# Kernel tuning notes

Measured on AMD Instinct MI355X. Metric: run time of the kernel, lower is better.

## Reference

```python
import jax, jax.numpy as jnp
import numpy as np

H, D = 8, 16            # heads, per-head dim (hidden_channels // heads)
HID = H * D             # 128
N_MAT, N_ELEM = 100000, 118
F_MAT, F_ELEM = 128, 64
OUT = 64
E_EM, E_MM = 1000000, 2000000
NEG_SLOPE = 0.2

def _k(i):
    return jax.random.fold_in(jax.random.key(0), i)

def setup_inputs() -> dict:
    p = lambda i, shape: 0.1 * jax.random.normal(_k(i), shape, dtype=jnp.float32)
    return dict(
        x_mat=jax.random.normal(_k(0), (N_MAT, F_MAT), dtype=jnp.float32),
        x_elem=jax.random.normal(_k(1), (N_ELEM, F_ELEM), dtype=jnp.float32),
        W_proj_mat=p(2, (HID, F_MAT)), b_proj_mat=p(3, (HID,)),
        W_proj_elem=p(4, (HID, F_ELEM)), b_proj_elem=p(5, (HID,)),
        a_src_em=p(6, (H, D)), a_dst_em=p(7, (H, D)),
        a_src_mm=p(8, (H, D)), a_dst_mm=p(9, (H, D)),
        Wk=p(10, (HID, HID)), bk=p(11, (HID,)), q=p(12, (HID,)),
        Wl=p(13, (OUT, HID)), bl=p(14, (OUT,)),
        src_em=jax.random.randint(_k(15), (E_EM,), 0, N_ELEM, dtype=jnp.int32),
        dst_em=jax.random.randint(_k(16), (E_EM,), 0, N_MAT, dtype=jnp.int32),
        src_mm=jax.random.randint(_k(17), (E_MM,), 0, N_MAT, dtype=jnp.int32),
        dst_mm=jax.random.randint(_k(18), (E_MM,), 0, N_MAT, dtype=jnp.int32),
    )

def _edge_type_conv(x_s, x_d, a_s, a_d, src, dst, n_dst):
    # x_s:[Ns,H,D], x_d:[Nd,H,D]; per-edge-type GAT-style attention (HANConv.message)
    alpha = jnp.sum(x_s * a_s, -1)[src] + jnp.sum(x_d * a_d, -1)[dst]   # [E,H]
    alpha = jax.nn.leaky_relu(alpha, NEG_SLOPE)
    amax = jax.ops.segment_max(alpha, dst, num_segments=n_dst)          # stable softmax per dst
    ex = jnp.exp(alpha - amax[dst])
    den = jax.ops.segment_sum(ex, dst, num_segments=n_dst)
    w = ex / (den[dst] + 1e-16)                                         # [E,H]
    out = jax.ops.segment_sum(x_s[src] * w[:, :, None], dst, num_segments=n_dst)  # [Nd,H,D]
    return jax.nn.relu(out.reshape(n_dst, HID))

def _group(xs, q, Wk, bk):
    # HANConv semantic-level attention over metapaths
    s = jnp.stack(xs)                                                   # [M,N,C]
    score = jnp.sum(q * jnp.mean(jnp.tanh(s @ Wk.T + bk), axis=1), axis=-1)  # [M]
    attn = jax.nn.softmax(score)
    return jnp.einsum('m,mnc->nc', attn, s)

def reference(x_mat, x_elem, W_proj_mat, b_proj_mat, W_proj_elem, b_proj_elem,
              a_src_em, a_dst_em, a_src_mm, a_dst_mm, Wk, bk, q, Wl, bl,
              src_em, dst_em, src_mm, dst_mm):
    h_mat = (x_mat @ W_proj_mat.T + b_proj_mat).reshape(N_MAT, H, D)
    h_elem = (x_elem @ W_proj_elem.T + b_proj_elem).reshape(N_ELEM, H, D)
    o_em = _edge_type_conv(h_elem, h_mat, a_src_em, a_dst_em, src_em, dst_em, N_MAT)
    o_mm = _edge_type_conv(h_mat, h_mat, a_src_mm, a_dst_mm, src_mm, dst_mm, N_MAT)
    out_mat = _group([o_em, o_mm], q, Wk, bk)                           # [N_MAT, HID]
    return out_mat @ Wl.T + bl                                          # final Linear
```

## Files before the change

### kernel.cpp

```cpp
#include <hip/hip_runtime.h>
#include <hip/hip_bf16.h>

typedef unsigned int uint32;
typedef unsigned short ushort16;

using bf16x8 = __attribute__((ext_vector_type(8))) short;
using f32x4  = __attribute__((ext_vector_type(4))) float;

#define N_MATN 100000
#define N_ELEMN 118
#define F_MATN 128
#define F_ELEMN 64
#define HIDN 128
#define NHEAD 8
#define OUTC 64
#define NSTRIPS 6250
#define NT2 16
#define NTILES2 (N_MATN/NT2)

#define SH 8
#define NBK 391
#define BCH 8192

__device__ __forceinline__ float blo(uint32 u){ return __uint_as_float(u << 16); }
__device__ __forceinline__ float bhi(uint32 u){ return __uint_as_float(u & 0xffff0000u); }
__device__ __forceinline__ ushort16 f2bf(float f){
    uint32 u = __float_as_uint(f);
    uint32 r = u + 0x7FFFu + ((u >> 16) & 1u);
    return (ushort16)(r >> 16);
}
__device__ __forceinline__ uint32 pack2(float a, float b){
    return (uint32)f2bf(a) | ((uint32)f2bf(b) << 16);
}
__device__ __forceinline__ bf16x8 cvt8(const float* __restrict__ p){
    bf16x8 r;
    #pragma unroll
    for(int j=0;j<8;j++) r[j] = (short)f2bf(p[j]);
    return r;
}

__global__ __launch_bounds__(256) void proj_all(
    const float* __restrict__ xe, const float* __restrict__ We,
    const float* __restrict__ be, const float* __restrict__ a_se,
    ushort16* __restrict__ h_elem, float* __restrict__ asrc_em,
    const float* __restrict__ x, const float* __restrict__ W,
    const float* __restrict__ bias,
    const float* __restrict__ a_de, const float* __restrict__ a_sm, const float* __restrict__ a_dm,
    ushort16* __restrict__ h,
    float* __restrict__ adst_em, float* __restrict__ asrc_mm, float* __restrict__ adst_mm)
{
    __shared__ float xr[F_ELEMN];
    int tid = threadIdx.x;
    if(blockIdx.x < N_ELEMN){
        int n = blockIdx.x, c = tid;
        if(c < 16) ((float4*)xr)[c] = ((const float4*)(xe + n*F_ELEMN))[c];
        __syncthreads();
        if(c < 128){
            const float4* Wr = (const float4*)(We + c*F_ELEMN);
            float acc = 0.f;
            #pragma unroll 4
            for(int i=0;i<16;i++){
                float4 w = Wr[i];
                acc += xr[4*i]*w.x + xr[4*i+1]*w.y + xr[4*i+2]*w.z + xr[4*i+3]*w.w;
            }
            acc += be[c];
            h_elem[n*HIDN + c] = f2bf(acc);
            float p = acc * a_se[c];
            #pragma unroll
            for(int m=8;m>=1;m>>=1) p += __shfl_xor(p, m, 16);
            if((c&15)==0) asrc_em[n*NHEAD + (c>>4)] = p;
        }
        return;
    }
    int wv = tid >> 6, lane = tid & 63, quad = lane >> 4, sl = lane & 15;
    bf16x8 B[2][4];
    float bc[2], ade[2], asv[2], adv[2];
    #pragma unroll
    for(int i=0;i<2;i++){
        int c = (2*wv+i)*16 + sl;
        const float* wr = W + c*F_MATN;
        #pragma unroll
        for(int ks=0;ks<4;ks++) B[i][ks] = cvt8(wr + ks*32 + quad*8);
        bc[i] = bias[c]; ade[i] = a_de[c]; asv[i] = a_sm[c]; adv[i] = a_dm[c];
    }
    int nb = gridDim.x - N_ELEMN;
    for(int s = blockIdx.x - N_ELEMN; s < NSTRIPS; s += nb){
        int n0 = s*16;
        const float* xrow = x + (size_t)(n0+sl)*F_MATN;
        bf16x8 A[4];
        #pragma unroll
        for(int ks=0;ks<4;ks++) A[ks] = cvt8(xrow + ks*32 + quad*8);
        f32x4 acc[2];
        #pragma unroll
        for(int i=0;i<2;i++){ acc[i][0]=0.f; acc[i][1]=0.f; acc[i][2]=0.f; acc[i][3]=0.f; }
        #pragma unroll
        for(int i=0;i<2;i++)
            #pragma unroll
            for(int ks=0;ks<4;ks++)
                acc[i] = __builtin_amdgcn_mfma_f32_16x16x32_bf16(A[ks], B[i][ks], acc[i], 0, 0, 0);
        #pragma unroll
        for(int i=0;i<2;i++){
            int head = 2*wv + i;
            #pragma unroll
            for(int r=0;r<4;r++){
                float a = acc[i][r] + bc[i];
                int node = n0 + quad*4 + r;
                h[(size_t)node*HIDN + head*16 + sl] = f2bf(a);
                float p0 = a*ade[i], p1 = a*asv[i], p2 = a*adv[i];
                #pragma unroll
                for(int m=8;m>=1;m>>=1){
                    p0 += __shfl_xor(p0, m);
                    p1 += __shfl_xor(p1, m);
                    p2 += __shfl_xor(p2, m);
                }
                if(sl == 0){
                    adst_em[node*NHEAD + head] = p0;
                    asrc_mm[node*NHEAD + head] = p1;
                    adst_mm[node*NHEAD + head] = p2;
                }
            }
        }
    }
}

__global__ __launch_bounds__(256) void bucket_count(
    const int* __restrict__ dst_em, int nE_em, int* __restrict__ bcnt_em,
    const int* __restrict__ dst_mm, int nE_mm, int* __restrict__ bcnt_mm)
{
    __shared__ int he[NBK], hm[NBK];
    int t = threadIdx.x;
    for(int i=t;i<NBK;i+=256){ he[i]=0; hm[i]=0; }
    __syncthreads();
    int gt = blockIdx.x*256 + t;
    int st = gridDim.x*256;
    {
        int n4 = nE_em >> 2;
        const int4* d4 = (const int4*)dst_em;
        for(int i = gt; i < n4; i += st){
            int4 v = d4[i];
            atomicAdd(&he[v.x>>SH],1); atomicAdd(&he[v.y>>SH],1);
            atomicAdd(&he[v.z>>SH],1); atomicAdd(&he[v.w>>SH],1);
        }
        for(int i = (n4<<2) + gt; i < nE_em; i += st) atomicAdd(&he[dst_em[i]>>SH],1);
    }
    {
        int n4 = nE_mm >> 2;
        const int4* d4 = (const int4*)dst_mm;
        for(int i = gt; i < n4; i += st){
            int4 v = d4[i];
            atomicAdd(&hm[v.x>>SH],1); atomicAdd(&hm[v.y>>SH],1);
            atomicAdd(&hm[v.z>>SH],1); atomicAdd(&hm[v.w>>SH],1);
        }
        for(int i = (n4<<2) + gt; i < nE_mm; i += st) atomicAdd(&hm[dst_mm[i]>>SH],1);
    }
    __syncthreads();
    for(int j=t;j<NBK;j+=256){
        int a = he[j], b = hm[j];
        if(a) atomicAdd(&bcnt_em[j], a);
        if(b) atomicAdd(&bcnt_mm[j], b);
    }
}

__global__ __launch_bounds__(512) void bucket_scan(
    const int* __restrict__ bcnt_em, int* __restrict__ bb_em, int* __restrict__ bcur_em,
    const int* __restrict__ bcnt_mm, int* __restrict__ bb_mm, int* __restrict__ bcur_mm,
    int* __restrict__ offs_em, int* __restrict__ offs_mm, int nE_em, int nE_mm)
{
    __shared__ int wsum[8];
    int t = threadIdx.x, l = t & 63, w = t >> 6;
    {
        int v = (t < NBK) ? bcnt_em[t] : 0;
        int x = v;
        #pragma unroll
        for(int off=1; off<64; off<<=1){ int y = __shfl_up(x, off); if(l >= off) x += y; }
        if(l == 63) wsum[w] = x;
        __syncthreads();
        int base = 0;
        for(int k=0;k<w;k++) base += wsum[k];
        int excl = base + x - v;
        if(t < NBK){ bb_em[t] = excl; bcur_em[t] = excl; }
        if(t == 0){ bb_em[NBK] = nE_em; offs_em[N_MATN] = nE_em; }
        __syncthreads();
    }
    {
        int v = (t < NBK) ? bcnt_mm[t] : 0;
        int x = v;
        #pragma unroll
        for(int off=1; off<64; off<<=1){ int y = __shfl_up(x, off); if(l >= off) x += y; }
        if(l == 63) wsum[w] = x;
        __syncthreads();
        int base = 0;
        for(int k=0;k<w;k++) base += wsum[k];
        int excl = base + x - v;
        if(t < NBK){ bb_mm[t] = excl; bcur_mm[t] = excl; }
        if(t == 0){ bb_mm[NBK] = nE_mm; offs_mm[N_MATN] = nE_mm; }
    }
}

__global__ __launch_bounds__(256) void bin_pass(
    const int* __restrict__ src_em, const int* __restrict__ dst_em, int nE_em,
    int* __restrict__ bcur_em, uint32* __restrict__ st_em,
    const int* __restrict__ src_mm, const int* __restrict__ dst_mm, int nE_mm,
    int* __restrict__ bcur_mm, uint32* __restrict__ st_mm)
{
    __shared__ int cnt[NBK];
    __shared__ int base[NBK];
    int t = threadIdx.x;
    int nch_em = (nE_em + BCH - 1)/BCH;
    int nch_mm = (nE_mm + BCH - 1)/BCH;
    int ntot = nch_em + nch_mm;
    for(int c = blockIdx.x; c < ntot; c += gridDim.x){
        bool em = c < nch_em;
        const int* src = em ? src_em : src_mm;
        const int* dst = em ? dst_em : dst_mm;
        int nE   = em ? nE_em : nE_mm;
        int* bcur = em ? bcur_em : bcur_mm;
        uint32* st = em ? st_em : st_mm;
        int cc = em ? c : c - nch_em;
        int s = cc*BCH;
        int e = s + BCH; if(e > nE) e = nE;
        int len = e - s;
        int n4 = len >> 2;
        const int4* d4 = (const int4*)(dst + s);
        const int4* s4 = (const int4*)(src + s);
        for(int i=t;i<NBK;i+=256) cnt[i] = 0;
        __syncthreads();
        for(int i=t;i<n4;i+=256){
            int4 v = d4[i];
            atomicAdd(&cnt[v.x>>SH],1); atomicAdd(&cnt[v.y>>SH],1);
            atomicAdd(&cnt[v.z>>SH],1); atomicAdd(&cnt[v.w>>SH],1);
        }
        for(int i = s + (n4<<2) + t; i < e; i += 256) atomicAdd(&cnt[dst[i]>>SH], 1);
        __syncthreads();
        for(int i=t;i<NBK;i+=256){
            int v = cnt[i];
            base[i] = v ? atomicAdd(&bcur[i], v) : 0;
            cnt[i] = 0;
        }
        __syncthreads();
        for(int i=t;i<n4;i+=256){
            int4 dv = d4[i];
            int4 sv = s4[i];
            int b, p;
            b = dv.x>>SH; p = base[b] + atomicAdd(&cnt[b],1);
            st[p] = ((uint32)(dv.x & ((1<<SH)-1)) << 17) | (uint32)sv.x;
            b = dv.y>>SH; p = base[b] + atomicAdd(&cnt[b],1);
            st[p] = ((uint32)(dv.y & ((1<<SH)-1)) << 17) | (uint32)sv.y;
            b = dv.z>>SH; p = base[b] + atomicAdd(&cnt[b],1);
            st[p] = ((uint32)(dv.z & ((1<<SH)-1)) << 17) | (uint32)sv.z;
            b = dv.w>>SH; p = base[b] + atomicAdd(&cnt[b],1);
            st[p] = ((uint32)(dv.w & ((1<<SH)-1)) << 17) | (uint32)sv.w;
        }
        for(int i = s + (n4<<2) + t; i < e; i += 256){
            int d = dst[i];
            int b = d >> SH;
            int p = base[b] + atomicAdd(&cnt[b], 1);
            st[p] = ((uint32)(d & ((1<<SH)-1)) << 17) | (uint32)src[i];
        }
        __syncthreads();
    }
}

__global__ __launch_bounds__(256) void place_pass(
    const int* __restrict__ bb_em, const uint32* __restrict__ st_em,
    int* __restrict__ csr_em, int* __restrict__ offs_em,
    const int* __restrict__ bb_mm, const uint32* __restrict__ st_mm,
    int* __restrict__ csr_mm, int* __restrict__ offs_mm)
{
    __shared__ int cnt[256];
    __shared__ int wsum[4];
    __shared__ int cur[256];
    int b = blockIdx.x;
    bool em = b < NBK;
    const int* bb        = em ? bb_em : bb_mm;
    const uint32* stp    = em ? st_em : st_mm;
    int* csr             = em ? csr_em : csr_mm;
    int* offs            = em ? offs_em : offs_mm;
    int bk = em ? b : b - NBK;
    int d0 = bk << SH;
    int t = threadIdx.x, l = t & 63, w = t >> 6;
    int nd = N_MATN - d0; if(nd > 256) nd = 256;
    int beg = bb[bk], end = bb[bk+1];
    cnt[t] = 0;
    __syncthreads();
    for(int i = beg + t; i < end; i += 256)
        atomicAdd(&cnt[stp[i] >> 17], 1);
    __syncthreads();
    int v = cnt[t];
    int x = v;
    #pragma unroll
    for(int off=1; off<64; off<<=1){ int y = __shfl_up(x, off); if(l >= off) x += y; }
    if(l == 63) wsum[w] = x;
    __syncthreads();
    int base = beg;
    for(int k=0;k<w;k++) base += wsum[k];
    int excl = base + x - v;
    cur[t] = excl;
    if(t < nd) offs[d0 + t] = excl;
    __syncthreads();
    for(int i = beg + t; i < end; i += 256){
        uint32 vv = stp[i];
        int dl = (int)(vv >> 17);
        int p = atomicAdd(&cur[dl], 1);
        csr[p] = (int)(vv & 0x1FFFFu);
    }
}

__global__ __launch_bounds__(256) void agg_both(
    const int* __restrict__ offs_em, const int* __restrict__ csr_em,
    const ushort16* __restrict__ h_elem, const float* __restrict__ asrc_em,
    const float* __restrict__ adst_em, ushort16* __restrict__ o_em,
    const int* __restrict__ offs_mm, const int* __restrict__ csr_mm,
    const ushort16* __restrict__ h_mat, const float* __restrict__ asrc_mm,
    const float* __restrict__ adst_mm, ushort16* __restrict__ o_mm)
{
    int lane = threadIdx.x & 63;
    int g = lane >> 4;
    int q = lane & 15;
    int hd = q >> 1;
    int w = (blockIdx.x*blockDim.x + threadIdx.x) >> 6;
    int nw = (gridDim.x*blockDim.x) >> 6;

    int begN = 0, endN = 0; float adN = 0.f;
    if(w < 2*N_MATN){
        int nid0 = __builtin_amdgcn_readfirstlane(w);
        bool em0 = nid0 < N_MATN;
        int dx = em0 ? nid0 : nid0 - N_MATN;
        const int* offsx = em0 ? offs_em : offs_mm;
        const float* adpx = em0 ? adst_em : adst_mm;
        begN = offsx[dx]; endN = offsx[dx+1];
        adN = adpx[(unsigned)(dx*NHEAD + hd)];
    }

    for(int nid = w; nid < 2*N_MATN; nid += nw){
        int nidu = __builtin_amdgcn_readfirstlane(nid);
        bool em = nidu < N_MATN;
        int d = em ? nidu : nidu - N_MATN;
        const int*    csr  = em ? csr_em  : csr_mm;
        const uint32* hs   = (const uint32*)(em ? h_elem : h_mat);
        const float*  asp  = em ? asrc_em : asrc_mm;
        uint32*       op   = (uint32*)(em ? o_em : o_mm);
        int beg = begN, end = endN;
        float ad = adN;
        int nxt = nidu + nw;
        if(nxt < 2*N_MATN){
            bool emx = nxt < N_MATN;
            int dx = emx ? nxt : nxt - N_MATN;
            const int* offsx = emx ? offs_em : offs_mm;
            const float* adpx = emx ? adst_em : adst_mm;
            begN = offsx[dx]; endN = offsx[dx+1];
            adN = adpx[(unsigned)(dx*NHEAD + hd)];
        }
        float denA = 0.f, denB = 0.f;
        float nloA[4] = {0.f,0.f,0.f,0.f}, nhiA[4] = {0.f,0.f,0.f,0.f};
        float nloB[4] = {0.f,0.f,0.f,0.f}, nhiB[4] = {0.f,0.f,0.f,0.f};
        for(int j0 = beg; j0 < end; j0 += 8){
            int e0 = j0 + 2*g, e1 = e0 + 1;
            bool v0 = e0 < end, v1 = e1 < end;
            int s0 = csr[(unsigned)(v0 ? e0 : end - 1)];
            int s1 = csr[(unsigned)(v1 ? e1 : end - 1)];
            float a0 = asp[(unsigned)(s0*NHEAD + hd)];
            float a1 = asp[(unsigned)(s1*NHEAD + hd)];
            const uint4 h0 = *(const uint4*)(hs + (unsigned)(s0*64 + q*4));
            const uint4 h1 = *(const uint4*)(hs + (unsigned)(s1*64 + q*4));
            float al0 = a0 + ad; al0 = fmaxf(al0, 0.2f*al0);
            float ex0 = __expf(al0); ex0 = v0 ? ex0 : 0.f;
            float al1 = a1 + ad; al1 = fmaxf(al1, 0.2f*al1);
            float ex1 = __expf(al1); ex1 = v1 ? ex1 : 0.f;
            denA += ex0; denB += ex1;
            nloA[0] += blo(h0.x)*ex0; nhiA[0] += bhi(h0.x)*ex0;
            nloA[1] += blo(h0.y)*ex0; nhiA[1] += bhi(h0.y)*ex0;
            nloA[2] += blo(h0.z)*ex0; nhiA[2] += bhi(h0.z)*ex0;
            nloA[3] += blo(h0.w)*ex0; nhiA[3] += bhi(h0.w)*ex0;
            nloB[0] += blo(h1.x)*ex1; nhiB[0] += bhi(h1.x)*ex1;
            nloB[1] += blo(h1.y)*ex1; nhiB[1] += bhi(h1.y)*ex1;
            nloB[2] += blo(h1.z)*ex1; nhiB[2] += bhi(h1.z)*ex1;
            nloB[3] += blo(h1.w)*ex1; nhiB[3] += bhi(h1.w)*ex1;
        }
        float den = denA + denB;
        den += __shfl_xor(den, 16); den += __shfl_xor(den, 32);
        float nlo[4], nhi[4];
        #pragma unroll
        for(int k=0;k<4;k++){
            nlo[k] = nloA[k] + nloB[k];
            nhi[k] = nhiA[k] + nhiB[k];
            nlo[k] += __shfl_xor(nlo[k], 16); nlo[k] += __shfl_xor(nlo[k], 32);
            nhi[k] += __shfl_xor(nhi[k], 16); nhi[k] += __shfl_xor(nhi[k], 32);
        }
        if(g == 0){
            float rdn = 1.0f/(den + 1e-16f);
            uint4 pk;
            pk.x = pack2(fmaxf(nlo[0]*rdn, 0.f), fmaxf(nhi[0]*rdn, 0.f));
            pk.y = pack2(fmaxf(nlo[1]*rdn, 0.f), fmaxf(nhi[1]*rdn, 0.f));
            pk.z = pack2(fmaxf(nlo[2]*rdn, 0.f), fmaxf(nhi[2]*rdn, 0.f));
            pk.w = pack2(fmaxf(nlo[3]*rdn, 0.f), fmaxf(nhi[3]*rdn, 0.f));
            *(uint4*)(op + (size_t)d*64 + q*4) = pk;
        }
    }
}

__global__ __launch_bounds__(256) void score_mfma(
    const ushort16* __restrict__ o_em, const ushort16* __restrict__ o_mm,
    const float* __restrict__ Wk, const float* __restrict__ bkv,
    const float* __restrict__ qv, float* __restrict__ scores)
{
    int tid = threadIdx.x;
    int wv = tid >> 6, lane = tid & 63, quad = lane >> 4, sl = lane & 15;
    bf16x8 B[2][4];
    float bkc[2], qc[2];
    #pragma unroll
    for(int i=0;i<2;i++){
        int c = (2*wv+i)*16 + sl;
        const float* wr = Wk + c*HIDN;
        #pragma unroll
        for(int ks=0;ks<4;ks++) B[i][ks] = cvt8(wr + ks*32 + quad*8);
        bkc[i] = bkv[c]; qc[i] = qv[c];
    }
    float se = 0.f, sm = 0.f;
    for(int s = blockIdx.x; s < NSTRIPS; s += gridDim.x){
        int n0 = s*16;
        const bf16x8* rowE = (const bf16x8*)(o_em + (size_t)(n0+sl)*HIDN);
        const bf16x8* rowM = (const bf16x8*)(o_mm + (size_t)(n0+sl)*HIDN);
        bf16x8 AE[4], AM[4];
        #pragma unroll
        for(int ks=0;ks<4;ks++){
            AE[ks] = rowE[ks*4 + quad];
            AM[ks] = rowM[ks*4 + quad];
        }
        f32x4 aE[2], aM[2];
        #pragma unroll
        for(int i=0;i<2;i++){
            aE[i][0]=0.f;aE[i][1]=0.f;aE[i][2]=0.f;aE[i][3]=0.f;
            aM[i][0]=0.f;aM[i][1]=0.f;aM[i][2]=0.f;aM[i][3]=0.f;
        }
        #pragma unroll
        for(int i=0;i<2;i++)
            #pragma unroll
            for(int ks=0;ks<4;ks++){
                aE[i] = __builtin_amdgcn_mfma_f32_16x16x32_bf16(AE[ks], B[i][ks], aE[i], 0, 0, 0);
                aM[i] = __builtin_amdgcn_mfma_f32_16x16x32_bf16(AM[ks], B[i][ks], aM[i], 0, 0, 0);
            }
        #pragma unroll
        for(int i=0;i<2;i++)
            #pragma unroll
            for(int r=0;r<4;r++){
                se += qc[i]*tanhf(aE[i][r] + bkc[i]);
                sm += qc[i]*tanhf(aM[i][r] + bkc[i]);
            }
    }
    #pragma unroll
    for(int m=32;m>=1;m>>=1){ se += __shfl_xor(se,m); sm += __shfl_xor(sm,m); }
    __shared__ float red[8];
    if(lane==0){ red[wv*2]=se; red[wv*2+1]=sm; }
    __syncthreads();
    if(tid==0){
        atomicAdd(&scores[0], red[0]+red[2]+red[4]+red[6]);
        atomicAdd(&scores[1], red[1]+red[3]+red[5]+red[7]);
    }
}

__global__ __launch_bounds__(256) void final_v4(
    const ushort16* __restrict__ o_em, const ushort16* __restrict__ o_mm,
    const float* __restrict__ Wl, const float* __restrict__ blv,
    const float* __restrict__ scores, float* __restrict__ out)
{
    __shared__ float wlds[64*129];
    __shared__ float zlds[NT2*128];
    int t = threadIdx.x;
    for(int i=t;i<2048;i+=256){
        float4 v = ((const float4*)Wl)[i];
        int r = i >> 5, k4 = i & 31;
        float* d = wlds + r*129 + k4*4;
        d[0]=v.x; d[1]=v.y; d[2]=v.z; d[3]=v.w;
    }
    float s0 = scores[0]*(1.0f/N_MATN), s1 = scores[1]*(1.0f/N_MATN);
    float mx = fmaxf(s0,s1);
    float e0 = __expf(s0-mx), e1 = __expf(s1-mx);
    float inv = 1.0f/(e0+e1);
    float a0 = e0*inv, a1 = e1*inv;
    int j = t & 63, half = t >> 6;
    float bj = blv[j];
    const float* wr = wlds + j*129;
    __syncthreads();
    for(int tile = blockIdx.x; tile < NTILES2; tile += gridDim.x){
        int n0 = tile*NT2;
        __syncthreads();
        {
            const uint4* pe = (const uint4*)((const uint32*)o_em + (size_t)n0*64);
            const uint4* pm = (const uint4*)((const uint32*)o_mm + (size_t)n0*64);
            uint4 ve = pe[t], vm = pm[t];
            float* zd = zlds + t*8;
            zd[0]=a0*blo(ve.x)+a1*blo(vm.x); zd[1]=a0*bhi(ve.x)+a1*bhi(vm.x);
            zd[2]=a0*blo(ve.y)+a1*blo(vm.y); zd[3]=a0*bhi(ve.y)+a1*bhi(vm.y);
            zd[4]=a0*blo(ve.z)+a1*blo(vm.z); zd[5]=a0*bhi(ve.z)+a1*bhi(vm.z);
            zd[6]=a0*blo(ve.w)+a1*blo(vm.w); zd[7]=a0*bhi(ve.w)+a1*bhi(vm.w);
        }
        __syncthreads();
        float acc[4] = {0.f,0.f,0.f,0.f};
        #pragma unroll 1
        for(int kk=0;kk<128;kk+=8){
            float f0=wr[kk],f1=wr[kk+1],f2=wr[kk+2],f3=wr[kk+3];
            float f4=wr[kk+4],f5=wr[kk+5],f6=wr[kk+6],f7=wr[kk+7];
            #pragma unroll
            for(int n=0;n<4;n++){
                const float4* zr = (const float4*)(zlds + (half*4+n)*128 + kk);
                float4 za = zr[0], zb = zr[1];
                acc[n] += za.x*f0 + za.y*f1 + za.z*f2 + za.w*f3
                        + zb.x*f4 + zb.y*f5 + zb.z*f6 + zb.w*f7;
            }
        }
        #pragma unroll
        for(int n=0;n<4;n++)
            out[(size_t)(n0 + half*4 + n)*OUTC + j] = bj + acc[n];
    }
}

extern "C" void kernel_launch(void* const* d_in, const int* in_sizes, int n_in,
                              void* d_out, int out_size, void* d_ws, size_t ws_size,
                              hipStream_t stream)
{
    const float* x_mat    = (const float*)d_in[0];
    const float* x_elem   = (const float*)d_in[1];
    const float* W_pm     = (const float*)d_in[2];
    const float* b_pm     = (const float*)d_in[3];
    const float* W_pe     = (const float*)d_in[4];
    const float* b_pe     = (const float*)d_in[5];
    const float* a_se     = (const float*)d_in[6];
    const float* a_de     = (const float*)d_in[7];
    const float* a_sm     = (const float*)d_in[8];
    const float* a_dm     = (const float*)d_in[9];
    const float* Wk       = (const float*)d_in[10];
    const float* bk       = (const float*)d_in[11];
    const float* qv       = (const float*)d_in[12];
    const float* Wl       = (const float*)d_in[13];
    const float* bl       = (const float*)d_in[14];
    const int* src_em     = (const int*)d_in[15];
    const int* dst_em     = (const int*)d_in[16];
    const int* src_mm     = (const int*)d_in[17];
    const int* dst_mm     = (const int*)d_in[18];
    int nE_em = in_sizes[15];
    int nE_mm = in_sizes[17];

    char* ws = (char*)d_ws;
    size_t off = 0;
    auto alloc = [&](size_t bytes) -> void* {
        void* p = ws + off; off += (bytes + 255) & ~size_t(255); return p;
    };
    ushort16* h_mat   = (ushort16*)alloc((size_t)N_MATN*HIDN*2);
    ushort16* h_elem  = (ushort16*)alloc((size_t)N_ELEMN*HIDN*2);
    float*    asrcEM  = (float*)   alloc((size_t)N_ELEMN*NHEAD*4);
    float*    adstEM  = (float*)   alloc((size_t)N_MATN*NHEAD*4);
    float*    asrcMM  = (float*)   alloc((size_t)N_MATN*NHEAD*4);
    float*    adstMM  = (float*)   alloc((size_t)N_MATN*NHEAD*4);
    int*      offs_em = (int*)     alloc((size_t)(N_MATN+1)*4);
    int*      offs_mm = (int*)     alloc((size_t)(N_MATN+1)*4);
    int*      csr_em  = (int*)     alloc((size_t)1000000*4);
    int*      csr_mm  = (int*)     alloc((size_t)2000000*4);
    ushort16* o_em    = (ushort16*)alloc((size_t)N_MATN*HIDN*2);
    ushort16* o_mm    = (ushort16*)alloc((size_t)N_MATN*HIDN*2);
    int*      bb_em   = (int*)     alloc((size_t)(NBK+1)*4);
    int*      bb_mm   = (int*)     alloc((size_t)(NBK+1)*4);
    int*      bcur_em = (int*)     alloc((size_t)NBK*4);
    int*      bcur_mm = (int*)     alloc((size_t)NBK*4);
    size_t zero_start = off;
    int*      bcnt_em = (int*)     alloc((size_t)NBK*4);
    int*      bcnt_mm = (int*)     alloc((size_t)NBK*4);
    float*    scores  = (float*)   alloc(256);
    size_t zero_bytes = off - zero_start;

    uint32* st_em = (uint32*)o_em;
    uint32* st_mm = st_em + nE_em;

    hipMemsetAsync(ws + zero_start, 0, zero_bytes, stream);

    proj_all<<<1024 + N_ELEMN, 256, 0, stream>>>(
        x_elem, W_pe, b_pe, a_se, h_elem, asrcEM,
        x_mat, W_pm, b_pm, a_de, a_sm, a_dm,
        h_mat, adstEM, asrcMM, adstMM);

    bucket_count<<<256, 256, 0, stream>>>(dst_em, nE_em, bcnt_em, dst_mm, nE_mm, bcnt_mm);
    bucket_scan<<<1, 512, 0, stream>>>(bcnt_em, bb_em, bcur_em,
                                       bcnt_mm, bb_mm, bcur_mm,
                                       offs_em, offs_mm, nE_em, nE_mm);

    int nch = (nE_em + BCH - 1)/BCH + (nE_mm + BCH - 1)/BCH;
    bin_pass<<<nch, 256, 0, stream>>>(src_em, dst_em, nE_em, bcur_em, st_em,
                                      src_mm, dst_mm, nE_mm, bcur_mm, st_mm);
    place_pass<<<2*NBK, 256, 0, stream>>>(bb_em, st_em, csr_em, offs_em,
                                          bb_mm, st_mm, csr_mm, offs_mm);

    agg_both<<<4096, 256, 0, stream>>>(offs_em, csr_em, h_elem, asrcEM, adstEM, o_em,
                                       offs_mm, csr_mm, h_mat, asrcMM, adstMM, o_mm);

    score_mfma<<<1024, 256, 0, stream>>>(o_em, o_mm, Wk, bk, qv, scores);
    final_v4<<<2048, 256, 0, stream>>>(o_em, o_mm, Wl, bl, scores, (float*)d_out);
}
```

Baseline: 476.5 us.

## Fuse bucket counting into projection kernel and simplify aggregation prefetch

Merges the bucket_count histogram pass into proj_all as an extra group of 128 blocks, so the projection and the destination counting run concurrently in one launch and one kernel boundary disappears. In agg_both it drops the software prefetch of the next node's offsets and attention term, loading them directly each iteration instead. It also changes the edge-to-lane assignment from adjacent pairs to a stride of four. The fused launch runs with fewer counting blocks than before, and removing the prefetch may expose load latency in the aggregation loop.

```diff
diff --git a/kernel.cpp b/kernel.cpp
--- a/kernel.cpp
+++ b/kernel.cpp
@@ -18,6 +18,9 @@
 #define NT2 16
 #define NTILES2 (N_MATN/NT2)
 
+#define MATBLK 1024
+#define CNTBLK 128
+
 #define SH 8
 #define NBK 391
 #define BCH 8192
@@ -47,11 +50,13 @@
     const float* __restrict__ bias,
     const float* __restrict__ a_de, const float* __restrict__ a_sm, const float* __restrict__ a_dm,
     ushort16* __restrict__ h,
-    float* __restrict__ adst_em, float* __restrict__ asrc_mm, float* __restrict__ adst_mm)
-{
-    __shared__ float xr[F_ELEMN];
+    float* __restrict__ adst_em, float* __restrict__ asrc_mm, float* __restrict__ adst_mm,
+    const int* __restrict__ dst_em, int nE_em, int* __restrict__ bcnt_em,
+    const int* __restrict__ dst_mm, int nE_mm, int* __restrict__ bcnt_mm)
+{
     int tid = threadIdx.x;
     if(blockIdx.x < N_ELEMN){
+        __shared__ float xr[F_ELEMN];
         int n = blockIdx.x, c = tid;
         if(c < 16) ((float4*)xr)[c] = ((const float4*)(xe + n*F_ELEMN))[c];
         __syncthreads();
@@ -72,6 +77,41 @@
         }
         return;
     }
+    if(blockIdx.x >= N_ELEMN + MATBLK){
+        __shared__ int he[NBK], hm[NBK];
+        for(int i=tid;i<NBK;i+=256){ he[i]=0; hm[i]=0; }
+        __syncthreads();
+        int cb = blockIdx.x - (N_ELEMN + MATBLK);
+        int gt = cb*256 + tid;
+        int st = CNTBLK*256;
+        {
+            int n4 = nE_em >> 2;
+            const int4* d4 = (const int4*)dst_em;
+            for(int i = gt; i < n4; i += st){
+                int4 v = d4[i];
+                atomicAdd(&he[v.x>>SH],1); atomicAdd(&he[v.y>>SH],1);
+                atomicAdd(&he[v.z>>SH],1); atomicAdd(&he[v.w>>SH],1);
+            }
+            for(int i = (n4<<2) + gt; i < nE_em; i += st) atomicAdd(&he[dst_em[i]>>SH],1);
+        }
+        {
+            int n4 = nE_mm >> 2;
+            const int4* d4 = (const int4*)dst_mm;
+            for(int i = gt; i < n4; i += st){
+                int4 v = d4[i];
+                atomicAdd(&hm[v.x>>SH],1); atomicAdd(&hm[v.y>>SH],1);
+                atomicAdd(&hm[v.z>>SH],1); atomicAdd(&hm[v.w>>SH],1);
+            }
+            for(int i = (n4<<2) + gt; i < nE_mm; i += st) atomicAdd(&hm[dst_mm[i]>>SH],1);
+        }
+        __syncthreads();
+        for(int j=tid;j<NBK;j+=256){
+            int a = he[j], b = hm[j];
+            if(a) atomicAdd(&bcnt_em[j], a);
+            if(b) atomicAdd(&bcnt_mm[j], b);
+        }
+        return;
+    }
     int wv = tid >> 6, lane = tid & 63, quad = lane >> 4, sl = lane & 15;
     bf16x8 B[2][4];
     float bc[2], ade[2], asv[2], adv[2];
@@ -83,8 +123,7 @@
         for(int ks=0;ks<4;ks++) B[i][ks] = cvt8(wr + ks*32 + quad*8);
         bc[i] = bias[c]; ade[i] = a_de[c]; asv[i] = a_sm[c]; adv[i] = a_dm[c];
     }
-    int nb = gridDim.x - N_ELEMN;
-    for(int s = blockIdx.x - N_ELEMN; s < NSTRIPS; s += nb){
+    for(int s = blockIdx.x - N_ELEMN; s < NSTRIPS; s += MATBLK){
         int n0 = s*16;
         const float* xrow = x + (size_t)(n0+sl)*F_MATN;
         bf16x8 A[4];
@@ -120,44 +159,6 @@
                 }
             }
         }
-    }
-}
-
-__global__ __launch_bounds__(256) void bucket_count(
-    const int* __restrict__ dst_em, int nE_em, int* __restrict__ bcnt_em,
-    const int* __restrict__ dst_mm, int nE_mm, int* __restrict__ bcnt_mm)
-{
-    __shared__ int he[NBK], hm[NBK];
-    int t = threadIdx.x;
-    for(int i=t;i<NBK;i+=256){ he[i]=0; hm[i]=0; }
-    __syncthreads();
-    int gt = blockIdx.x*256 + t;
-    int st = gridDim.x*256;
-    {
-        int n4 = nE_em >> 2;
-        const int4* d4 = (const int4*)dst_em;
-        for(int i = gt; i < n4; i += st){
-            int4 v = d4[i];
-            atomicAdd(&he[v.x>>SH],1); atomicAdd(&he[v.y>>SH],1);
-            atomicAdd(&he[v.z>>SH],1); atomicAdd(&he[v.w>>SH],1);
-        }
-        for(int i = (n4<<2) + gt; i < nE_em; i += st) atomicAdd(&he[dst_em[i]>>SH],1);
-    }
-    {
-        int n4 = nE_mm >> 2;
-        const int4* d4 = (const int4*)dst_mm;
-        for(int i = gt; i < n4; i += st){
-            int4 v = d4[i];
-            atomicAdd(&hm[v.x>>SH],1); atomicAdd(&hm[v.y>>SH],1);
-            atomicAdd(&hm[v.z>>SH],1); atomicAdd(&hm[v.w>>SH],1);
-        }
-        for(int i = (n4<<2) + gt; i < nE_mm; i += st) atomicAdd(&hm[dst_mm[i]>>SH],1);
-    }
-    __syncthreads();
-    for(int j=t;j<NBK;j+=256){
-        int a = he[j], b = hm[j];
-        if(a) atomicAdd(&bcnt_em[j], a);
-        if(b) atomicAdd(&bcnt_mm[j], b);
     }
 }
 
@@ -320,42 +321,23 @@
     int hd = q >> 1;
     int w = (blockIdx.x*blockDim.x + threadIdx.x) >> 6;
     int nw = (gridDim.x*blockDim.x) >> 6;
-
-    int begN = 0, endN = 0; float adN = 0.f;
-    if(w < 2*N_MATN){
-        int nid0 = __builtin_amdgcn_readfirstlane(w);
-        bool em0 = nid0 < N_MATN;
-        int dx = em0 ? nid0 : nid0 - N_MATN;
-        const int* offsx = em0 ? offs_em : offs_mm;
-        const float* adpx = em0 ? adst_em : adst_mm;
-        begN = offsx[dx]; endN = offsx[dx+1];
-        adN = adpx[(unsigned)(dx*NHEAD + hd)];
-    }
-
     for(int nid = w; nid < 2*N_MATN; nid += nw){
         int nidu = __builtin_amdgcn_readfirstlane(nid);
         bool em = nidu < N_MATN;
         int d = em ? nidu : nidu - N_MATN;
+        const int*    offs = em ? offs_em : offs_mm;
         const int*    csr  = em ? csr_em  : csr_mm;
         const uint32* hs   = (const uint32*)(em ? h_elem : h_mat);
         const float*  asp  = em ? asrc_em : asrc_mm;
+        const float*  adp  = em ? adst_em : adst_mm;
         uint32*       op   = (uint32*)(em ? o_em : o_mm);
-        int beg = begN, end = endN;
-        float ad = adN;
-        int nxt = nidu + nw;
-        if(nxt < 2*N_MATN){
-            bool emx = nxt < N_MATN;
-            int dx = emx ? nxt : nxt - N_MATN;
-            const int* offsx = emx ? offs_em : offs_mm;
-            const float* adpx = emx ? adst_em : adst_mm;
-            begN = offsx[dx]; endN = offsx[dx+1];
-            adN = adpx[(unsigned)(dx*NHEAD + hd)];
-        }
+        int beg = offs[d], end = offs[d+1];
+        float ad = adp[(unsigned)(d*NHEAD + hd)];
         float denA = 0.f, denB = 0.f;
         float nloA[4] = {0.f,0.f,0.f,0.f}, nhiA[4] = {0.f,0.f,0.f,0.f};
         float nloB[4] = {0.f,0.f,0.f,0.f}, nhiB[4] = {0.f,0.f,0.f,0.f};
         for(int j0 = beg; j0 < end; j0 += 8){
-            int e0 = j0 + 2*g, e1 = e0 + 1;
+            int e0 = j0 + g, e1 = j0 + 4 + g;
             bool v0 = e0 < end, v1 = e1 < end;
             int s0 = csr[(unsigned)(v0 ? e0 : end - 1)];
             int s1 = csr[(unsigned)(v1 ? e1 : end - 1)];
@@ -573,12 +555,12 @@
 
     hipMemsetAsync(ws + zero_start, 0, zero_bytes, stream);
 
-    proj_all<<<1024 + N_ELEMN, 256, 0, stream>>>(
+    proj_all<<<N_ELEMN + MATBLK + CNTBLK, 256, 0, stream>>>(
         x_elem, W_pe, b_pe, a_se, h_elem, asrcEM,
         x_mat, W_pm, b_pm, a_de, a_sm, a_dm,
-        h_mat, adstEM, asrcMM, adstMM);
-
-    bucket_count<<<256, 256, 0, stream>>>(dst_em, nE_em, bcnt_em, dst_mm, nE_mm, bcnt_mm);
+        h_mat, adstEM, asrcMM, adstMM,
+        dst_em, nE_em, bcnt_em, dst_mm, nE_mm, bcnt_mm);
+
     bucket_scan<<<1, 512, 0, stream>>>(bcnt_em, bb_em, bcur_em,
                                        bcnt_mm, bb_mm, bcur_mm,
                                        offs_em, offs_mm, nE_em, nE_mm);
```

Result: no change. 468.3 us (-1.7%).
